# Optimization experiments

Hardware: AMD Instinct MI355X
Metric: run time of the kernel (lower is better)

Reference implementation:

```python
import jax, jax.numpy as jnp
import numpy as np

WIN = 7          # gaussian window size (odd)
SIGMA = 1.5
DOWNSCALE = 2
C1 = 0.01 ** 2
C2 = 0.03 ** 2


def _gauss_window(dtype):
    x = jnp.arange(WIN, dtype=jnp.float32) - (WIN - 1) / 2
    g = jnp.exp(-x ** 2 / (2 * SIGMA ** 2))
    g = g / g.sum()
    w2d = jnp.outer(g, g)                      # (7,7)
    return w2d[None, None].astype(dtype)       # OIHW = (1,1,7,7)


def _avg_pool(x, k):
    if k == 1:
        return x
    s = jax.lax.reduce_window(x, 0.0, jax.lax.add,
                              (1, 1, k, k), (1, 1, k, k), 'VALID')
    return s / (k * k)


def _blur(x, w):
    pad = WIN // 2
    return jax.lax.conv_general_dilated(
        x, w, window_strides=(1, 1),
        padding=[(pad, pad), (pad, pad)],
        dimension_numbers=('NCHW', 'OIHW', 'NCHW'))


def setup_inputs() -> dict:
    key = jax.random.key(0)
    k1, k2 = jax.random.split(key)
    shape = (16, 1, 768, 1024)
    pred = jax.random.uniform(k1, shape, dtype=jnp.float32)
    target = jax.random.uniform(k2, shape, dtype=jnp.float32)
    return {"pred": pred, "target": target}


def reference(pred, target):
    p = _avg_pool(pred, DOWNSCALE)
    t = _avg_pool(target, DOWNSCALE)
    w = _gauss_window(p.dtype)

    mu1 = _blur(p, w)
    mu2 = _blur(t, w)
    mu1_sq = mu1 * mu1
    mu2_sq = mu2 * mu2
    mu1_mu2 = mu1 * mu2

    sigma1_sq = _blur(p * p, w) - mu1_sq
    sigma2_sq = _blur(t * t, w) - mu2_sq
    sigma12 = _blur(p * t, w) - mu1_mu2

    num = (2 * mu1_mu2 + C1) * (2 * sigma12 + C2)
    den = (mu1_sq + mu2_sq + C1) * (sigma1_sq + sigma2_sq + C2)
    ssim_map = num / (den + 1e-12)
    return 1.0 - ssim_map.mean()
```

## Files before the change

kernel.cpp:

```cpp
#include <hip/hip_runtime.h>
#include <math.h>

#define NIMG 16
#define IH 768
#define IW 1024
#define HD 384
#define WD 512
#define TH 16
#define TW 64
#define HALO_Y 3
#define HALO_X 4
#define RH (TH + 2*HALO_Y)
#define RW (TW + 2*HALO_X)
#define NPAIR (RW/2)
#define NSLOT (RH*NPAIR)
#define NGX (WD/TW)
#define NGY (HD/TH)
#define NBLK (NGX*NGY*NIMG)
#define SSIM_C1 1.0e-4f
#define SSIM_C2 9.0e-4f

struct GW { float g[7]; };

__global__ __launch_bounds__(256, 5) void ssim_main(
    const float* __restrict__ pred, const float* __restrict__ tgt,
    float* __restrict__ partial, GW gw)
{
  __shared__ float p_s[RH][RW];
  __shared__ float t_s[RH][RW];
  __shared__ float wred[4];

  const int tid = threadIdx.x;
  const int bx = blockIdx.x, by = blockIdx.y, n = blockIdx.z;
  const int tx0 = bx * TW, ty0 = by * TH;
  const float* __restrict__ pb = pred + (size_t)n * IH * IW;
  const float* __restrict__ tb = tgt  + (size_t)n * IH * IW;

#pragma unroll
  for (int i = 0; i < 4; ++i) {
    const int slot = tid + i * 256;
    if (slot < NSLOT) {
      const int row  = slot / NPAIR;
      const int pair = slot - row * NPAIR;
      const int gy = ty0 + row - HALO_Y;
      const int pg = tx0 + 2 * pair - HALO_X;
      float pv0 = 0.f, pv1 = 0.f, tv0 = 0.f, tv1 = 0.f;
      if ((unsigned)gy < (unsigned)HD && (unsigned)pg < (unsigned)WD) {
        const size_t o0 = (size_t)(2 * gy) * IW + (size_t)(2 * pg);
        const float4 a = *(const float4*)(pb + o0);
        const float4 b = *(const float4*)(pb + o0 + IW);
        const float4 c = *(const float4*)(tb + o0);
        const float4 d = *(const float4*)(tb + o0 + IW);
        pv0 = 0.25f * ((a.x + a.y) + (b.x + b.y));
        pv1 = 0.25f * ((a.z + a.w) + (b.z + b.w));
        tv0 = 0.25f * ((c.x + c.y) + (d.x + d.y));
        tv1 = 0.25f * ((c.z + c.w) + (d.z + d.w));
      }
      *(float2*)&p_s[row][2 * pair] = make_float2(pv0, pv1);
      *(float2*)&t_s[row][2 * pair] = make_float2(tv0, tv1);
    }
  }
  __syncthreads();

  const int y  = tid >> 4;
  const int c0 = (tid & 15) << 2;

  float a1[12], a2[12], app[12], att[12], apt[12];
#pragma unroll
  for (int i = 0; i < 12; ++i) { a1[i]=0.f; a2[i]=0.f; app[i]=0.f; att[i]=0.f; apt[i]=0.f; }

#pragma unroll
  for (int k = 0; k < 7; ++k) {
    const float w = gw.g[k];
#pragma unroll
    for (int g = 0; g < 3; ++g) {
      const float4 P = *(const float4*)&p_s[y + k][c0 + 4 * g];
      const float4 T = *(const float4*)&t_s[y + k][c0 + 4 * g];
      const int b = 4 * g;
      a1[b+0] = fmaf(w, P.x, a1[b+0]);  a1[b+1] = fmaf(w, P.y, a1[b+1]);
      a1[b+2] = fmaf(w, P.z, a1[b+2]);  a1[b+3] = fmaf(w, P.w, a1[b+3]);
      a2[b+0] = fmaf(w, T.x, a2[b+0]);  a2[b+1] = fmaf(w, T.y, a2[b+1]);
      a2[b+2] = fmaf(w, T.z, a2[b+2]);  a2[b+3] = fmaf(w, T.w, a2[b+3]);
      app[b+0] = fmaf(w, P.x*P.x, app[b+0]);  app[b+1] = fmaf(w, P.y*P.y, app[b+1]);
      app[b+2] = fmaf(w, P.z*P.z, app[b+2]);  app[b+3] = fmaf(w, P.w*P.w, app[b+3]);
      att[b+0] = fmaf(w, T.x*T.x, att[b+0]);  att[b+1] = fmaf(w, T.y*T.y, att[b+1]);
      att[b+2] = fmaf(w, T.z*T.z, att[b+2]);  att[b+3] = fmaf(w, T.w*T.w, att[b+3]);
      apt[b+0] = fmaf(w, P.x*T.x, apt[b+0]);  apt[b+1] = fmaf(w, P.y*T.y, apt[b+1]);
      apt[b+2] = fmaf(w, P.z*T.z, apt[b+2]);  apt[b+3] = fmaf(w, P.w*T.w, apt[b+3]);
    }
  }

  float lsum = 0.f;
#pragma unroll
  for (int j = 0; j < 4; ++j) {
    float mu1 = 0.f, mu2 = 0.f, bpp = 0.f, btt = 0.f, bpt = 0.f;
#pragma unroll
    for (int k = 0; k < 7; ++k) {
      const float w = gw.g[k];
      const int idx = j + 1 + k;
      mu1 = fmaf(w, a1[idx],  mu1);
      mu2 = fmaf(w, a2[idx],  mu2);
      bpp = fmaf(w, app[idx], bpp);
      btt = fmaf(w, att[idx], btt);
      bpt = fmaf(w, apt[idx], bpt);
    }
    const float mu1sq = mu1 * mu1;
    const float mu2sq = mu2 * mu2;
    const float mu12  = mu1 * mu2;
    const float s1    = bpp - mu1sq;
    const float s2    = btt - mu2sq;
    const float s12   = bpt - mu12;
    const float num = (2.f * mu12 + SSIM_C1) * (2.f * s12 + SSIM_C2);
    const float den = (mu1sq + mu2sq + SSIM_C1) * (s1 + s2 + SSIM_C2);
    lsum += num / (den + 1e-12f);
  }

#pragma unroll
  for (int off = 32; off > 0; off >>= 1)
    lsum += __shfl_down(lsum, off, 64);
  if ((tid & 63) == 0) wred[tid >> 6] = lsum;
  __syncthreads();
  if (tid == 0)
    partial[((size_t)n * NGY + by) * NGX + bx] =
        wred[0] + wred[1] + wred[2] + wred[3];
}

__global__ __launch_bounds__(256) void ssim_final(
    const float* __restrict__ partial, float* __restrict__ out)
{
  __shared__ float red[4];
  float s = 0.f;
  for (int i = threadIdx.x; i < NBLK; i += 256) s += partial[i];
#pragma unroll
  for (int off = 32; off > 0; off >>= 1)
    s += __shfl_down(s, off, 64);
  if ((threadIdx.x & 63) == 0) red[threadIdx.x >> 6] = s;
  __syncthreads();
  if (threadIdx.x == 0) {
    const float tot = red[0] + red[1] + red[2] + red[3];
    out[0] = 1.0f - tot * (1.0f / (float)((size_t)NIMG * HD * WD));
  }
}

extern "C" void kernel_launch(void* const* d_in, const int* in_sizes, int n_in,
                              void* d_out, int out_size, void* d_ws, size_t ws_size,
                              hipStream_t stream) {
  const float* pred = (const float*)d_in[0];
  const float* tgt  = (const float*)d_in[1];
  float* out     = (float*)d_out;
  float* partial = (float*)d_ws;

  GW gw;
  double gd[7], s = 0.0;
  for (int i = 0; i < 7; ++i) {
    const double x = (double)i - 3.0;
    gd[i] = exp(-x * x / (2.0 * 1.5 * 1.5));
    s += gd[i];
  }
  for (int i = 0; i < 7; ++i) gw.g[i] = (float)(gd[i] / s);

  dim3 grid(NGX, NGY, NIMG);
  ssim_main<<<grid, 256, 0, stream>>>(pred, tgt, partial, gw);
  ssim_final<<<1, 256, 0, stream>>>(partial, out);
}
```

Baseline: 134.2 us.

## Restructure SSIM blur as horizontal-first pass with column-per-lane mapping

The thread mapping changes so each wave owns 4 output rows and each lane owns one column. Each lane computes a 7-tap horizontal blur of the five moment maps over 10 shared-memory rows, then folds those into vertical accumulators for its 4 outputs. The shared tile row stride is padded to 74 floats, and the occupancy hint drops from 5 to 4 blocks. The aim is to cut redundant blur arithmetic and register pressure. The cost is many more scalar LDS reads in place of the earlier float4 reads.

```diff
diff --git a/kernel.cpp b/kernel.cpp
--- a/kernel.cpp
+++ b/kernel.cpp
@@ -12,6 +12,7 @@
 #define HALO_X 4
 #define RH (TH + 2*HALO_Y)
 #define RW (TW + 2*HALO_X)
+#define RWS 74
 #define NPAIR (RW/2)
 #define NSLOT (RH*NPAIR)
 #define NGX (WD/TW)
@@ -22,12 +23,12 @@
 
 struct GW { float g[7]; };
 
-__global__ __launch_bounds__(256, 5) void ssim_main(
+__global__ __launch_bounds__(256, 4) void ssim_main(
     const float* __restrict__ pred, const float* __restrict__ tgt,
     float* __restrict__ partial, GW gw)
 {
-  __shared__ float p_s[RH][RW];
-  __shared__ float t_s[RH][RW];
+  __shared__ float p_s[RH][RWS];
+  __shared__ float t_s[RH][RWS];
   __shared__ float wred[4];
 
   const int tid = threadIdx.x;
@@ -62,54 +63,58 @@
   }
   __syncthreads();
 
-  const int y  = tid >> 4;
-  const int c0 = (tid & 15) << 2;
+  const int lane = tid & 63;
+  const int wv   = tid >> 6;
+  const int r0   = wv * 4;
+  const int c    = lane;
 
-  float a1[12], a2[12], app[12], att[12], apt[12];
+  float acc0[4], acc1[4], acc2[4], acc3[4], acc4[4];
 #pragma unroll
-  for (int i = 0; i < 12; ++i) { a1[i]=0.f; a2[i]=0.f; app[i]=0.f; att[i]=0.f; apt[i]=0.f; }
+  for (int r = 0; r < 4; ++r) { acc0[r]=0.f; acc1[r]=0.f; acc2[r]=0.f; acc3[r]=0.f; acc4[r]=0.f; }
 
 #pragma unroll
-  for (int k = 0; k < 7; ++k) {
-    const float w = gw.g[k];
+  for (int j = 0; j < 10; ++j) {
+    const int lrow = r0 + j;
+    const float* __restrict__ prow = &p_s[lrow][c + 1];
+    const float* __restrict__ trow = &t_s[lrow][c + 1];
+    float hp = 0.f, ht = 0.f, hpp = 0.f, htt = 0.f, hpt = 0.f;
 #pragma unroll
-    for (int g = 0; g < 3; ++g) {
-      const float4 P = *(const float4*)&p_s[y + k][c0 + 4 * g];
-      const float4 T = *(const float4*)&t_s[y + k][c0 + 4 * g];
-      const int b = 4 * g;
-      a1[b+0] = fmaf(w, P.x, a1[b+0]);  a1[b+1] = fmaf(w, P.y, a1[b+1]);
-      a1[b+2] = fmaf(w, P.z, a1[b+2]);  a1[b+3] = fmaf(w, P.w, a1[b+3]);
-      a2[b+0] = fmaf(w, T.x, a2[b+0]);  a2[b+1] = fmaf(w, T.y, a2[b+1]);
-      a2[b+2] = fmaf(w, T.z, a2[b+2]);  a2[b+3] = fmaf(w, T.w, a2[b+3]);
-      app[b+0] = fmaf(w, P.x*P.x, app[b+0]);  app[b+1] = fmaf(w, P.y*P.y, app[b+1]);
-      app[b+2] = fmaf(w, P.z*P.z, app[b+2]);  app[b+3] = fmaf(w, P.w*P.w, app[b+3]);
-      att[b+0] = fmaf(w, T.x*T.x, att[b+0]);  att[b+1] = fmaf(w, T.y*T.y, att[b+1]);
-      att[b+2] = fmaf(w, T.z*T.z, att[b+2]);  att[b+3] = fmaf(w, T.w*T.w, att[b+3]);
-      apt[b+0] = fmaf(w, P.x*T.x, apt[b+0]);  apt[b+1] = fmaf(w, P.y*T.y, apt[b+1]);
-      apt[b+2] = fmaf(w, P.z*T.z, apt[b+2]);  apt[b+3] = fmaf(w, P.w*T.w, apt[b+3]);
+    for (int k = 0; k < 7; ++k) {
+      const float wk = gw.g[k];
+      const float p = prow[k];
+      const float t = trow[k];
+      const float wp = wk * p;
+      const float wt = wk * t;
+      hp += wp;
+      ht += wt;
+      hpp = fmaf(wp, p, hpp);
+      htt = fmaf(wt, t, htt);
+      hpt = fmaf(wp, t, hpt);
+    }
+#pragma unroll
+    for (int r = 0; r < 4; ++r) {
+      const int ki = j - r;
+      if (ki >= 0 && ki < 7) {
+        const float wvk = gw.g[ki];
+        acc0[r] = fmaf(wvk, hp,  acc0[r]);
+        acc1[r] = fmaf(wvk, ht,  acc1[r]);
+        acc2[r] = fmaf(wvk, hpp, acc2[r]);
+        acc3[r] = fmaf(wvk, htt, acc3[r]);
+        acc4[r] = fmaf(wvk, hpt, acc4[r]);
+      }
     }
   }
 
   float lsum = 0.f;
 #pragma unroll
-  for (int j = 0; j < 4; ++j) {
-    float mu1 = 0.f, mu2 = 0.f, bpp = 0.f, btt = 0.f, bpt = 0.f;
-#pragma unroll
-    for (int k = 0; k < 7; ++k) {
-      const float w = gw.g[k];
-      const int idx = j + 1 + k;
-      mu1 = fmaf(w, a1[idx],  mu1);
-      mu2 = fmaf(w, a2[idx],  mu2);
-      bpp = fmaf(w, app[idx], bpp);
-      btt = fmaf(w, att[idx], btt);
-      bpt = fmaf(w, apt[idx], bpt);
-    }
+  for (int r = 0; r < 4; ++r) {
+    const float mu1 = acc0[r], mu2 = acc1[r];
     const float mu1sq = mu1 * mu1;
     const float mu2sq = mu2 * mu2;
     const float mu12  = mu1 * mu2;
-    const float s1    = bpp - mu1sq;
-    const float s2    = btt - mu2sq;
-    const float s12   = bpt - mu12;
+    const float s1    = acc2[r] - mu1sq;
+    const float s2    = acc3[r] - mu2sq;
+    const float s12   = acc4[r] - mu12;
     const float num = (2.f * mu12 + SSIM_C1) * (2.f * s12 + SSIM_C2);
     const float den = (mu1sq + mu2sq + SSIM_C1) * (s1 + s2 + SSIM_C2);
     lsum += num / (den + 1e-12f);
@@ -118,7 +123,7 @@
 #pragma unroll
   for (int off = 32; off > 0; off >>= 1)
     lsum += __shfl_down(lsum, off, 64);
-  if ((tid & 63) == 0) wred[tid >> 6] = lsum;
+  if (lane == 0) wred[wv] = lsum;
   __syncthreads();
   if (tid == 0)
     partial[((size_t)n * NGY + by) * NGX + bx] =
```

Result: faster. 127.4 us (-5.0%).
